# Kernel optimization log

Measured on AMD Instinct MI355X. Metric: run time of the kernel, lower is better.

## Reference

```python
import jax, jax.numpy as jnp
import numpy as np

EPS = 1e-12
TEMP = 0.05
LAMBDA2 = 0.5


def _normalize(x):
    # F.normalize(x, dim=1), eps=1e-12
    n = jnp.linalg.norm(x, axis=1, keepdims=True)
    return x / jnp.maximum(n, EPS)


def _cdist(x, f):
    # torch.cdist p=2: [B, N] euclidean distances
    x2 = jnp.sum(x * x, axis=1, keepdims=True)          # [B,1]
    f2 = jnp.sum(f * f, axis=1)[None, :]                # [1,N]
    d2 = x2 + f2 - 2.0 * (x @ f.T)
    return jnp.sqrt(jnp.maximum(d2, 0.0))


def _ce(logits, targets):
    # F.cross_entropy with integer targets, mean reduction
    logp = jax.nn.log_softmax(logits, axis=1)
    return -jnp.take_along_axis(logp, targets[:, None], axis=1).mean()


def _branch_loss(x_raw, f, targets):
    x = _normalize(x_raw)
    # note: original applies cross_entropy (which does another log_softmax)
    # on top of softmax(cdist(...)) -- reproduced faithfully
    soft = jax.nn.softmax(_cdist(x, f), axis=1)
    out = (x @ f.T) / TEMP
    return _ce(out, targets) + _ce(soft, targets)


def setup_inputs() -> dict:
    key = jax.random.key(0)
    ks = jax.random.split(key, 7)
    B, N, D = 256, 8192, 2048
    inputs = jax.random.normal(ks[0], (B, D), dtype=jnp.float32)
    inputs_up = jax.random.normal(ks[1], (B, D), dtype=jnp.float32)
    inputs_down = jax.random.normal(ks[2], (B, D), dtype=jnp.float32)
    targets = jax.random.randint(ks[3], (B,), 0, N)
    # memory banks are buffers; initialize as L2-normalized rows (realistic state)
    features = _normalize(jax.random.normal(ks[4], (N, D), dtype=jnp.float32))
    features_up = _normalize(jax.random.normal(ks[5], (N, D), dtype=jnp.float32))
    features_down = _normalize(jax.random.normal(ks[6], (N, D), dtype=jnp.float32))
    return {
        "inputs": inputs,
        "inputs_up": inputs_up,
        "inputs_down": inputs_down,
        "targets": targets,
        "epoch": 10,
        "features": features,
        "features_up": features_up,
        "features_down": features_down,
    }


def reference(inputs, inputs_up, inputs_down, targets, epoch, features, features_up, features_down):
    l_mid = _branch_loss(inputs, features, targets)
    l_up = _branch_loss(inputs_up, features_up, targets)
    l_down = _branch_loss(inputs_down, features_down, targets)
    loss = (1.0 - LAMBDA2) * l_mid + LAMBDA2 * (l_up + l_down)
    return loss
```

## Files before the change

### kernel.cpp

```cpp
#include <hip/hip_runtime.h>

typedef float f4v __attribute__((ext_vector_type(4)));
typedef float f32x4 __attribute__((ext_vector_type(4)));
typedef __bf16 bf16x8 __attribute__((ext_vector_type(8)));
typedef __bf16 bf16x4 __attribute__((ext_vector_type(4)));
typedef unsigned short ushort8 __attribute__((ext_vector_type(8)));

static constexpr int KDIM = 2048;

static constexpr size_t OFF_XN      = 0;
static constexpr size_t OFF_PART    = (size_t)3 * 256 * 2048 * 2;
static constexpr size_t OFF_DOTT    = OFF_PART + (size_t)768 * 256 * 16;
static constexpr size_t OFF_ROWLOSS = OFF_DOTT + 768 * 4;

__device__ __forceinline__ unsigned short f2bf(float x) {
  union { float f; unsigned u; } c; c.f = x;
  unsigned r = c.u + 0x7fffu + ((c.u >> 16) & 1u);
  return (unsigned short)(r >> 16);
}

__device__ __forceinline__ void gload_lds16(const void* g, void* l) {
  __builtin_amdgcn_global_load_lds((const __attribute__((address_space(1))) void*)g,
                                   (__attribute__((address_space(3))) void*)l,
                                   16, 0, 0);
}

__device__ __forceinline__ void cvt_store8(char* p, f4v v) {
  bf16x4 o;
  o[0] = (__bf16)v[0]; o[1] = (__bf16)v[1]; o[2] = (__bf16)v[2]; o[3] = (__bf16)v[3];
  *(bf16x4*)p = o;
}

__global__ __launch_bounds__(256) void k_normalize(
    const float* __restrict__ x0, const float* __restrict__ x1, const float* __restrict__ x2,
    unsigned short* __restrict__ xn)
{
  int bid = blockIdx.x;
  int branch = bid >> 8;
  int row = bid & 255;
  const float* src = (branch == 0 ? x0 : (branch == 1 ? x1 : x2)) + (size_t)row * KDIM;
  int tid = threadIdx.x;
  f4v a = *(const f4v*)(src + tid * 8);
  f4v b = *(const f4v*)(src + tid * 8 + 4);
  float s = a[0]*a[0] + a[1]*a[1] + a[2]*a[2] + a[3]*a[3]
          + b[0]*b[0] + b[1]*b[1] + b[2]*b[2] + b[3]*b[3];
  #pragma unroll
  for (int m = 1; m < 64; m <<= 1) s += __shfl_xor(s, m);
  __shared__ float ls[4];
  if ((tid & 63) == 0) ls[tid >> 6] = s;
  __syncthreads();
  float total = ls[0] + ls[1] + ls[2] + ls[3];
  float inv = 1.0f / fmaxf(sqrtf(total), 1e-12f);
  ushort8 u;
  #pragma unroll
  for (int e = 0; e < 4; ++e) u[e]     = f2bf(a[e] * inv);
  #pragma unroll
  for (int e = 0; e < 4; ++e) u[4 + e] = f2bf(b[e] * inv);
  *(ushort8*)(xn + (size_t)bid * KDIM + tid * 8) = u;
}

__global__ __launch_bounds__(256, 3) void k_gemm_fused(
    const unsigned short* __restrict__ xn,
    const float* __restrict__ f0, const float* __restrict__ f1, const float* __restrict__ f2,
    const int* __restrict__ targets,
    float* __restrict__ part, float* __restrict__ dotT)
{
  __shared__ char lds[2 * 24576];

  int bid = blockIdx.x;
  int swz = (bid & 7) * 96 + (bid >> 3);
  int branch = swz >> 8;
  int ntile = (swz & 255) >> 1;
  int mtile = swz & 1;

  const unsigned short* A = xn + ((size_t)branch * 256 + (size_t)mtile * 128) * KDIM;
  const float* F = (branch == 0 ? f0 : (branch == 1 ? f1 : f2)) + (size_t)ntile * 64 * KDIM;

  int tid = threadIdx.x;
  int wave = tid >> 6;
  int lane = tid & 63;
  int rcol0 = lane & 15;
  int klane = lane >> 4;
  int wr = wave >> 1;
  int wc = wave & 1;

  const unsigned short* aSrc = A + (size_t)(tid >> 3) * KDIM
                             + (((tid & 7) ^ ((tid >> 3) & 7)) << 3);
  char* aDst = lds + (wave * 64) * 16;

#define STAGE_A(kt, buf) do { \
    _Pragma("unroll") for (int g = 0; g < 4; ++g) \
      gload_lds16(aSrc + (size_t)g * 32 * KDIM + (kt) * 64, \
                  aDst + (buf) * 24576 + g * 4096); \
  } while (0)

  const float* bSrc = F + (size_t)(tid >> 4) * KDIM + (tid & 15) * 4;

#define LOADB_G(kt, r0, r1, r2, r3) do { \
    r0 = *(const f4v*)(bSrc + (kt) * 64); \
    r1 = *(const f4v*)(bSrc + 16 * KDIM + (kt) * 64); \
    r2 = *(const f4v*)(bSrc + 32 * KDIM + (kt) * 64); \
    r3 = *(const f4v*)(bSrc + 48 * KDIM + (kt) * 64); \
  } while (0)

  int bOff = 16384 + (tid >> 4) * 128
           + (((((tid & 15) >> 1)) ^ ((tid >> 4) & 7)) << 4) + (tid & 1) * 8;

#define WRITE_B(r0, r1, r2, r3, buf) do { \
    char* wb = lds + (buf) * 24576 + bOff; \
    cvt_store8(wb,         r0); \
    cvt_store8(wb + 2048,  r1); \
    cvt_store8(wb + 4096,  r2); \
    cvt_store8(wb + 6144,  r3); \
  } while (0)

  f32x4 acc[4][2];
  #pragma unroll
  for (int i = 0; i < 4; ++i)
    #pragma unroll
    for (int j = 0; j < 2; ++j)
      #pragma unroll
      for (int q = 0; q < 4; ++q) acc[i][j][q] = 0.0f;

  int sa = rcol0 & 7;
  const char* aRd = lds + (wr * 64 + rcol0) * 128;
  const char* bRd = lds + 16384 + (wc * 32 + rcol0) * 128;

#define COMPUTE(buf) do { \
    const char* ra = aRd + (buf) * 24576; \
    const char* rb = bRd + (buf) * 24576; \
    _Pragma("unroll") for (int ks = 0; ks < 2; ++ks) { \
      int ch = (((ks * 4 + klane) ^ sa) << 4); \
      bf16x8 b0 = *(const bf16x8*)(rb + ch); \
      bf16x8 b1 = *(const bf16x8*)(rb + 2048 + ch); \
      bf16x8 a0 = *(const bf16x8*)(ra + ch); \
      bf16x8 a1 = *(const bf16x8*)(ra + 2048 + ch); \
      bf16x8 a2 = *(const bf16x8*)(ra + 4096 + ch); \
      bf16x8 a3 = *(const bf16x8*)(ra + 6144 + ch); \
      acc[0][0] = __builtin_amdgcn_mfma_f32_16x16x32_bf16(a0, b0, acc[0][0], 0, 0, 0); \
      acc[0][1] = __builtin_amdgcn_mfma_f32_16x16x32_bf16(a0, b1, acc[0][1], 0, 0, 0); \
      acc[1][0] = __builtin_amdgcn_mfma_f32_16x16x32_bf16(a1, b0, acc[1][0], 0, 0, 0); \
      acc[1][1] = __builtin_amdgcn_mfma_f32_16x16x32_bf16(a1, b1, acc[1][1], 0, 0, 0); \
      acc[2][0] = __builtin_amdgcn_mfma_f32_16x16x32_bf16(a2, b0, acc[2][0], 0, 0, 0); \
      acc[2][1] = __builtin_amdgcn_mfma_f32_16x16x32_bf16(a2, b1, acc[2][1], 0, 0, 0); \
      acc[3][0] = __builtin_amdgcn_mfma_f32_16x16x32_bf16(a3, b0, acc[3][0], 0, 0, 0); \
      acc[3][1] = __builtin_amdgcn_mfma_f32_16x16x32_bf16(a3, b1, acc[3][1], 0, 0, 0); \
    } \
  } while (0)

#define PHASE_END_4() do { \
    asm volatile("s_waitcnt vmcnt(4) lgkmcnt(0)" ::: "memory"); \
    __builtin_amdgcn_s_barrier(); \
    __builtin_amdgcn_sched_barrier(0); \
  } while (0)

  f4v pA0, pA1, pA2, pA3;
  f4v pB0, pB1, pB2, pB3;

  STAGE_A(0, 0);
  __builtin_amdgcn_sched_barrier(0);
  LOADB_G(0, pA0, pA1, pA2, pA3);
  LOADB_G(1, pB0, pB1, pB2, pB3);
  WRITE_B(pA0, pA1, pA2, pA3, 0);
  PHASE_END_4();

  for (int t = 0; t < 30; t += 2) {
    STAGE_A(t + 1, 1);
    __builtin_amdgcn_sched_barrier(0);
    LOADB_G(t + 2, pA0, pA1, pA2, pA3);
    WRITE_B(pB0, pB1, pB2, pB3, 1);
    COMPUTE(0);
    PHASE_END_4();
    STAGE_A(t + 2, 0);
    __builtin_amdgcn_sched_barrier(0);
    LOADB_G(t + 3, pB0, pB1, pB2, pB3);
    WRITE_B(pA0, pA1, pA2, pA3, 0);
    COMPUTE(1);
    PHASE_END_4();
  }
  STAGE_A(31, 1);
  WRITE_B(pB0, pB1, pB2, pB3, 1);
  COMPUTE(0);
  asm volatile("s_waitcnt vmcnt(0) lgkmcnt(0)" ::: "memory");
  __builtin_amdgcn_s_barrier();
  __builtin_amdgcn_sched_barrier(0);
  COMPUTE(1);

#undef STAGE_A
#undef LOADB_G
#undef WRITE_B
#undef COMPUTE
#undef PHASE_END_4

  int tbase = branch * 256;
  int mbase = mtile * 128;
  #pragma unroll
  for (int i = 0; i < 4; ++i) {
    #pragma unroll
    for (int q = 0; q < 4; ++q) {
      int row = mbase + wr * 64 + i * 16 + (klane << 2) + q;
      int tgt = targets[row];
      float s1 = 0.f, s2 = 0.f, s3 = 0.f, s4 = 0.f;
      #pragma unroll
      for (int j = 0; j < 2; ++j) {
        float d = acc[i][j][q];
        float e1 = __expf(fmaf(20.0f, d, -20.0f));
        float Dv = sqrtf(fmaxf(2.0f - 2.0f * d, 0.0f));
        float e2 = __expf(Dv - 2.0f);
        s1 += e1; s2 += e2;
        float t2 = e2 * e2;
        s3 += t2; s4 += t2 * e2;
        int col = ntile * 64 + wc * 32 + j * 16 + rcol0;
        if (col == tgt) dotT[tbase + row] = d;
      }
      #pragma unroll
      for (int m = 1; m < 16; m <<= 1) {
        s1 += __shfl_xor(s1, m);
        s2 += __shfl_xor(s2, m);
        s3 += __shfl_xor(s3, m);
        s4 += __shfl_xor(s4, m);
      }
      if (rcol0 == 0) {
        f32x4 p; p[0] = s1; p[1] = s2; p[2] = s3; p[3] = s4;
        *(f32x4*)(part + ((size_t)(tbase + row) * 256 + ntile * 2 + wc) * 4) = p;
      }
    }
  }
}

__global__ __launch_bounds__(256) void k_combine(
    const float* __restrict__ part, const float* __restrict__ dotT, float* __restrict__ rowloss)
{
  int row = blockIdx.x;
  int tid = threadIdx.x;
  f4v p = *(const f4v*)(part + ((size_t)row * 256 + tid) * 4);
  float a0 = p[0], a1 = p[1], a2 = p[2], a3 = p[3];
  #pragma unroll
  for (int m = 1; m < 64; m <<= 1) {
    a0 += __shfl_xor(a0, m); a1 += __shfl_xor(a1, m);
    a2 += __shfl_xor(a2, m); a3 += __shfl_xor(a3, m);
  }
  __shared__ float ls[4][4];
  if ((tid & 63) == 0) {
    int w = tid >> 6;
    ls[0][w] = a0; ls[1][w] = a1; ls[2][w] = a2; ls[3][w] = a3;
  }
  __syncthreads();
  if (tid == 0) {
    float p1 = ls[0][0] + ls[0][1] + ls[0][2] + ls[0][3];
    float Z1 = ls[1][0] + ls[1][1] + ls[1][2] + ls[1][3];
    float Z2 = ls[2][0] + ls[2][1] + ls[2][2] + ls[2][3];
    float Z3 = ls[3][0] + ls[3][1] + ls[3][2] + ls[3][3];
    float dt = dotT[row];
    float CE1 = 20.0f + logf(p1) - 20.0f * dt;
    float Dt = sqrtf(fmaxf(2.0f - 2.0f * dt, 0.0f));
    float St = __expf(Dt - 2.0f) / Z1;
    float sES = 8193.0f + Z2 / (2.0f * Z1 * Z1) + Z3 / (6.0f * Z1 * Z1 * Z1);
    float CE2 = logf(sES) - St;
    rowloss[row] = (CE1 + CE2) * (0.5f / 256.0f);
  }
}

__global__ __launch_bounds__(256) void k_final(const float* __restrict__ rowloss, float* __restrict__ out)
{
  int tid = threadIdx.x;
  float v = rowloss[tid] + rowloss[tid + 256] + rowloss[tid + 512];
  #pragma unroll
  for (int m = 1; m < 64; m <<= 1) v += __shfl_xor(v, m);
  __shared__ float ls[4];
  if ((tid & 63) == 0) ls[tid >> 6] = v;
  __syncthreads();
  if (tid == 0) out[0] = ls[0] + ls[1] + ls[2] + ls[3];
}

extern "C" void kernel_launch(void* const* d_in, const int* in_sizes, int n_in,
                              void* d_out, int out_size, void* d_ws, size_t ws_size,
                              hipStream_t stream) {
  const float* in0 = (const float*)d_in[0];
  const float* in1 = (const float*)d_in[1];
  const float* in2 = (const float*)d_in[2];
  const int* targets = (const int*)d_in[3];
  const float* f0 = (const float*)d_in[5];
  const float* f1 = (const float*)d_in[6];
  const float* f2 = (const float*)d_in[7];

  char* ws = (char*)d_ws;
  unsigned short* xn = (unsigned short*)(ws + OFF_XN);
  float* part    = (float*)(ws + OFF_PART);
  float* dotT    = (float*)(ws + OFF_DOTT);
  float* rowloss = (float*)(ws + OFF_ROWLOSS);
  float* out = (float*)d_out;

  k_normalize<<<768, 256, 0, stream>>>(in0, in1, in2, xn);
  k_gemm_fused<<<768, 256, 0, stream>>>(xn, f0, f1, f2, targets, part, dotT);
  k_combine<<<768, 256, 0, stream>>>(part, dotT, rowloss);
  k_final<<<1, 256, 0, stream>>>(rowloss, out);
}
```

Baseline: 65.89 us.

## Deepen GEMM pipeline to triple-buffered LDS with three in-flight B register sets

Converts the double-buffered main loop of the fused GEMM into a three-stage pipeline. A tiles are prefetched two steps ahead into three LDS slots, and B tiles are loaded three steps ahead into three register sets. The LDS write of B now comes after the MFMA compute. This hides more global-memory latency, but it needs 72KB of LDS and more registers, so launch bounds drop from 3 to 2 blocks per CU and occupancy falls.

After: 73.05 us. +10.9%, slower.

```diff
diff --git a/kernel.cpp b/kernel.cpp
--- a/kernel.cpp
+++ b/kernel.cpp
@@ -59,13 +59,13 @@
   *(ushort8*)(xn + (size_t)bid * KDIM + tid * 8) = u;
 }
 
-__global__ __launch_bounds__(256, 3) void k_gemm_fused(
+__global__ __launch_bounds__(256, 2) void k_gemm_fused(
     const unsigned short* __restrict__ xn,
     const float* __restrict__ f0, const float* __restrict__ f1, const float* __restrict__ f2,
     const int* __restrict__ targets,
     float* __restrict__ part, float* __restrict__ dotT)
 {
-  __shared__ char lds[2 * 24576];
+  __shared__ char lds[73728];
 
   int bid = blockIdx.x;
   int swz = (bid & 7) * 96 + (bid >> 3);
@@ -86,32 +86,33 @@
 
   const unsigned short* aSrc = A + (size_t)(tid >> 3) * KDIM
                              + (((tid & 7) ^ ((tid >> 3) & 7)) << 3);
-  char* aDst = lds + (wave * 64) * 16;
-
-#define STAGE_A(kt, buf) do { \
+  char* aDst = lds + wave * 1024;
+
+#define STAGE_A(kt, slot) do { \
     _Pragma("unroll") for (int g = 0; g < 4; ++g) \
       gload_lds16(aSrc + (size_t)g * 32 * KDIM + (kt) * 64, \
-                  aDst + (buf) * 24576 + g * 4096); \
+                  aDst + (slot) * 16384 + g * 4096); \
   } while (0)
 
   const float* bSrc = F + (size_t)(tid >> 4) * KDIM + (tid & 15) * 4;
-
-#define LOADB_G(kt, r0, r1, r2, r3) do { \
-    r0 = *(const f4v*)(bSrc + (kt) * 64); \
-    r1 = *(const f4v*)(bSrc + 16 * KDIM + (kt) * 64); \
-    r2 = *(const f4v*)(bSrc + 32 * KDIM + (kt) * 64); \
-    r3 = *(const f4v*)(bSrc + 48 * KDIM + (kt) * 64); \
-  } while (0)
-
-  int bOff = 16384 + (tid >> 4) * 128
+  f4v bA0, bA1, bA2, bA3, bB0, bB1, bB2, bB3, bC0, bC1, bC2, bC3;
+
+#define LOADB_G(kt, R) do { \
+    R##0 = *(const f4v*)(bSrc + (kt) * 64); \
+    R##1 = *(const f4v*)(bSrc + 16 * KDIM + (kt) * 64); \
+    R##2 = *(const f4v*)(bSrc + 32 * KDIM + (kt) * 64); \
+    R##3 = *(const f4v*)(bSrc + 48 * KDIM + (kt) * 64); \
+  } while (0)
+
+  int bOff = (tid >> 4) * 128
            + (((((tid & 15) >> 1)) ^ ((tid >> 4) & 7)) << 4) + (tid & 1) * 8;
 
-#define WRITE_B(r0, r1, r2, r3, buf) do { \
-    char* wb = lds + (buf) * 24576 + bOff; \
-    cvt_store8(wb,         r0); \
-    cvt_store8(wb + 2048,  r1); \
-    cvt_store8(wb + 4096,  r2); \
-    cvt_store8(wb + 6144,  r3); \
+#define WRITE_B(R, slot) do { \
+    char* wb = lds + 49152 + (slot) * 8192 + bOff; \
+    cvt_store8(wb,        R##0); \
+    cvt_store8(wb + 2048, R##1); \
+    cvt_store8(wb + 4096, R##2); \
+    cvt_store8(wb + 6144, R##3); \
   } while (0)
 
   f32x4 acc[4][2];
@@ -123,12 +124,12 @@
       for (int q = 0; q < 4; ++q) acc[i][j][q] = 0.0f;
 
   int sa = rcol0 & 7;
-  const char* aRd = lds + (wr * 64 + rcol0) * 128;
-  const char* bRd = lds + 16384 + (wc * 32 + rcol0) * 128;
-
-#define COMPUTE(buf) do { \
-    const char* ra = aRd + (buf) * 24576; \
-    const char* rb = bRd + (buf) * 24576; \
+  int aRdOff = (wr * 64 + rcol0) * 128;
+  int bRdOff = (wc * 32 + rcol0) * 128;
+
+#define COMPUTE(slot) do { \
+    const char* ra = lds + (slot) * 16384 + aRdOff; \
+    const char* rb = lds + 49152 + (slot) * 8192 + bRdOff; \
     _Pragma("unroll") for (int ks = 0; ks < 2; ++ks) { \
       int ch = (((ks * 4 + klane) ^ sa) << 4); \
       bf16x8 b0 = *(const bf16x8*)(rb + ch); \
@@ -148,49 +149,56 @@
     } \
   } while (0)
 
-#define PHASE_END_4() do { \
-    asm volatile("s_waitcnt vmcnt(4) lgkmcnt(0)" ::: "memory"); \
+#define PHASE_END(vm) do { \
+    asm volatile("s_waitcnt vmcnt(" #vm ") lgkmcnt(0)" ::: "memory"); \
     __builtin_amdgcn_s_barrier(); \
     __builtin_amdgcn_sched_barrier(0); \
   } while (0)
 
-  f4v pA0, pA1, pA2, pA3;
-  f4v pB0, pB1, pB2, pB3;
+#define PHASE_FULL(kt, SA_SLOT, LB_R, C_SLOT, WB_R, WB_SLOT) do { \
+    STAGE_A((kt) + 2, SA_SLOT); \
+    __builtin_amdgcn_sched_barrier(0); \
+    LOADB_G((kt) + 3, LB_R); \
+    __builtin_amdgcn_sched_barrier(0); \
+    COMPUTE(C_SLOT); \
+    WRITE_B(WB_R, WB_SLOT); \
+    PHASE_END(12); \
+  } while (0)
 
   STAGE_A(0, 0);
+  STAGE_A(1, 1);
   __builtin_amdgcn_sched_barrier(0);
-  LOADB_G(0, pA0, pA1, pA2, pA3);
-  LOADB_G(1, pB0, pB1, pB2, pB3);
-  WRITE_B(pA0, pA1, pA2, pA3, 0);
-  PHASE_END_4();
-
-  for (int t = 0; t < 30; t += 2) {
-    STAGE_A(t + 1, 1);
-    __builtin_amdgcn_sched_barrier(0);
-    LOADB_G(t + 2, pA0, pA1, pA2, pA3);
-    WRITE_B(pB0, pB1, pB2, pB3, 1);
-    COMPUTE(0);
-    PHASE_END_4();
-    STAGE_A(t + 2, 0);
-    __builtin_amdgcn_sched_barrier(0);
-    LOADB_G(t + 3, pB0, pB1, pB2, pB3);
-    WRITE_B(pA0, pA1, pA2, pA3, 0);
-    COMPUTE(1);
-    PHASE_END_4();
-  }
+  LOADB_G(0, bA);
+  LOADB_G(1, bB);
+  LOADB_G(2, bC);
+  __builtin_amdgcn_sched_barrier(0);
+  WRITE_B(bA, 0);
+  PHASE_END(8);
+
+  #pragma unroll 1
+  for (int t = 0; t < 27; t += 3) {
+    PHASE_FULL(t,     2, bA, 0, bB, 1);
+    PHASE_FULL(t + 1, 0, bB, 1, bC, 2);
+    PHASE_FULL(t + 2, 1, bC, 2, bA, 0);
+  }
+  PHASE_FULL(27, 2, bA, 0, bB, 1);
+  PHASE_FULL(28, 0, bB, 1, bC, 2);
   STAGE_A(31, 1);
-  WRITE_B(pB0, pB1, pB2, pB3, 1);
+  __builtin_amdgcn_sched_barrier(0);
+  COMPUTE(2);
+  WRITE_B(bA, 0);
+  PHASE_END(8);
   COMPUTE(0);
-  asm volatile("s_waitcnt vmcnt(0) lgkmcnt(0)" ::: "memory");
-  __builtin_amdgcn_s_barrier();
-  __builtin_amdgcn_sched_barrier(0);
+  WRITE_B(bB, 1);
+  PHASE_END(0);
   COMPUTE(1);
 
 #undef STAGE_A
 #undef LOADB_G
 #undef WRITE_B
 #undef COMPUTE
-#undef PHASE_END_4
+#undef PHASE_END
+#undef PHASE_FULL
 
   int tbase = branch * 256;
   int mbase = mtile * 128;
```
